# Optimization experiments

Hardware: AMD Instinct MI355X
Metric: run time of the kernel (lower is better)

The kernel has to match this reference:

```python
import jax, jax.numpy as jnp
import numpy as np
import math

B, S, N_STATE = 2, 2048, 2048
N_HEAD, D_HEAD = 16, 128
NEG = -1e9


def rope(x, f_r, f_i):
    # x: [B,S,H,D], f_*: [B,S,1,D//2]
    x_r, x_i = jnp.split(x, 2, axis=-1)
    return jnp.concatenate([x_r * f_r - x_i * f_i, x_r * f_i + x_i * f_r], axis=-1)


def setup_inputs() -> dict:
    key = jax.random.key(0)
    ks = jax.random.split(key, 6)
    x = jax.random.normal(ks[0], (B, S, N_STATE), jnp.float32)
    # rotary freqs: cos/sin of standard RoPE angles
    inv_freq = 1.0 / (10000.0 ** (jnp.arange(0, D_HEAD, 2, dtype=jnp.float32) / D_HEAD))
    ang = jnp.arange(S, dtype=jnp.float32)[:, None] * inv_freq[None, :]  # [S, D/2]
    f_r = jnp.broadcast_to(jnp.cos(ang)[None, :, None, :], (B, S, 1, D_HEAD // 2))
    f_i = jnp.broadcast_to(jnp.sin(ang)[None, :, None, :], (B, S, 1, D_HEAD // 2))
    # causal additive mask: 0 on/below diagonal, -1e9 above
    causal = jnp.where(jnp.tril(jnp.ones((S, S), bool)), 0.0, NEG).astype(jnp.float32)
    attention_mask = jnp.broadcast_to(causal[None], (B, S, S))
    std = 1.0 / math.sqrt(N_STATE)
    W_qkv = jax.random.normal(ks[1], (3 * N_HEAD * D_HEAD, N_STATE), jnp.float32) * std
    b_qkv = jax.random.normal(ks[2], (3 * N_HEAD * D_HEAD,), jnp.float32) * 0.02
    W_o = jax.random.normal(ks[3], (N_STATE, N_HEAD * D_HEAD), jnp.float32) * std
    return {"x": x, "f_r": f_r, "f_i": f_i, "attention_mask": attention_mask,
            "W_qkv": W_qkv, "b_qkv": b_qkv, "W_o": W_o}


def reference(x, f_r, f_i, attention_mask, W_qkv, b_qkv, W_o):
    nb, ns, _ = x.shape
    qkv = x @ W_qkv.T + b_qkv  # [B,S,3*H*D]
    q, k, v = jnp.split(qkv, 3, axis=-1)
    q = rope(q.reshape(nb, ns, N_HEAD, D_HEAD), f_r, f_i)
    k = rope(k.reshape(nb, ns, N_HEAD, D_HEAD), f_r, f_i)
    v = v.reshape(nb, ns, N_HEAD, D_HEAD)
    # kv_cache=None: cache is just (k, v)
    qk = jnp.einsum("bqhd,bkhd->bhqk", q, k) / math.sqrt(D_HEAD)
    qk = qk + attention_mask[:, None, :, :]
    scores = jax.nn.softmax(qk.astype(jnp.float32), axis=-1).astype(x.dtype)
    out = jnp.einsum("bhqk,bkhd->bqhd", scores, v).reshape(nb, ns, N_HEAD * D_HEAD)
    out = out @ W_o.T
    return out, k, v
```

## Files before the change

### kernel.cpp

```cpp
#include <hip/hip_runtime.h>
#include <stdint.h>

#define BS   2
#define SS   2048
#define NH   16
#define DH   128
#define HD   2048
#define KDIM 2048
#define NT   32

typedef _Float16 half_t;
typedef _Float16 half8 __attribute__((ext_vector_type(8)));
typedef _Float16 half4v __attribute__((ext_vector_type(4)));
typedef float   float4_ __attribute__((ext_vector_type(4)));

__device__ __forceinline__ void async16(const void* g, void* l) {
  __builtin_amdgcn_global_load_lds(
      (__attribute__((address_space(1))) void*)(void*)g,
      (__attribute__((address_space(3))) void*)l,
      16, 0, 0);
}

#define XN4  2097152
#define WQ4  3145728
#define WO4  1048576
__global__ __launch_bounds__(256) void conv_all(const float* __restrict__ x,
                                                const float* __restrict__ Wqkv,
                                                const float* __restrict__ Wo,
                                                half_t* __restrict__ xh,
                                                half_t* __restrict__ wqh,
                                                half_t* __restrict__ woh) {
  int i = blockIdx.x * 256 + threadIdx.x;
  const float* src; half_t* dst; int o;
  if (i < XN4)            { src = x;    dst = xh;  o = i; }
  else if (i < XN4 + WQ4) { src = Wqkv; dst = wqh; o = i - XN4; }
  else                    { src = Wo;   dst = woh; o = i - XN4 - WQ4; }
  float4 v = ((const float4*)src)[o];
  half4v hv;
  hv.x = (half_t)v.x; hv.y = (half_t)v.y; hv.z = (half_t)v.z; hv.w = (half_t)v.w;
  ((half4v*)dst)[o] = hv;
}


__device__ __forceinline__ const half8* lds_frag(const half_t* l, int row, int j) {
  return (const half8*)&l[(row * 8 + (j ^ (row & 7))) * 8];
}

__device__ __forceinline__ void stage8(const half_t* __restrict__ Ab,
                                       const half_t* __restrict__ Wb,
                                       half_t* dA, half_t* dB, int k0,
                                       int wave, int lane) {
#pragma unroll
  for (int i = 0; i < 4; ++i) {
    int p = (wave * 4 + i) * 64 + lane;
    int r = p >> 3, j = (p & 7) ^ ((p >> 3) & 7);
    async16(Ab + (size_t)r * KDIM + k0 + j * 8, &dA[p * 8]);
    async16(Wb + (size_t)r * KDIM + k0 + j * 8, &dB[p * 8]);
  }
}

__device__ __forceinline__ void gemm_core(const half_t* __restrict__ Ab,
                                          const half_t* __restrict__ Wb,
                                          half_t* lA, half_t* lB,
                                          float4_ acc[4][4]) {
  const int tid = threadIdx.x, wave = tid >> 6, lane = tid & 63;
  const int quad = lane >> 4, tl = lane & 15;
  const int wm = wave >> 1, wn = wave & 1;

  stage8(Ab, Wb, lA, lB, 0, wave, lane);
  stage8(Ab, Wb, lA + 8192, lB + 8192, 64, wave, lane);

  for (int t = 0; t < NT; ++t) {
    if (t == NT - 1) asm volatile("s_waitcnt vmcnt(0)" ::: "memory");
    else             asm volatile("s_waitcnt vmcnt(8)" ::: "memory");
    __builtin_amdgcn_s_barrier();

    const half_t* cA = lA + (t & 1) * 8192;
    const half_t* cB = lB + (t & 1) * 8192;
    half8 af[4][2], bf[4][2];
#pragma unroll
    for (int ks = 0; ks < 2; ++ks) {
#pragma unroll
      for (int mi = 0; mi < 4; ++mi)
        af[mi][ks] = *lds_frag(cA, wm * 64 + mi * 16 + tl, ks * 4 + quad);
#pragma unroll
      for (int ni = 0; ni < 4; ++ni)
        bf[ni][ks] = *lds_frag(cB, wn * 64 + ni * 16 + tl, ks * 4 + quad);
    }
    asm volatile("s_waitcnt lgkmcnt(0)" ::: "memory");
    __builtin_amdgcn_sched_barrier(0);
    __builtin_amdgcn_s_barrier();

    if (t + 2 < NT)
      stage8(Ab, Wb, lA + (t & 1) * 8192, lB + (t & 1) * 8192,
             (t + 2) * 64, wave, lane);
    __builtin_amdgcn_sched_barrier(0);

    __builtin_amdgcn_s_setprio(1);
#pragma unroll
    for (int mi = 0; mi < 4; ++mi)
#pragma unroll
      for (int ni = 0; ni < 4; ++ni)
#pragma unroll
        for (int ks = 0; ks < 2; ++ks)
          acc[mi][ni] = __builtin_amdgcn_mfma_f32_16x16x32_f16(
              af[mi][ks], bf[ni][ks], acc[mi][ni], 0, 0, 0);
    __builtin_amdgcn_s_setprio(0);
  }
}

__global__ __launch_bounds__(256) void gemm_qkv(const half_t* __restrict__ A,
                                                const half_t* __restrict__ W,
                                                const float* __restrict__ bias,
                                                half_t* __restrict__ qh,
                                                half_t* __restrict__ kh,
                                                half_t* __restrict__ vh,
                                                float* __restrict__ vout) {
  __shared__ __align__(16) half_t lA[2 * 128 * 64];
  __shared__ __align__(16) half_t lB[2 * 128 * 64];
  const int tid = threadIdx.x, wave = tid >> 6, lane = tid & 63;
  const int quad = lane >> 4, tl = lane & 15;
  const int wm = wave >> 1, wn = wave & 1;
  const int bm = blockIdx.y * 128, bn = blockIdx.x * 128;

  float4_ acc[4][4];
#pragma unroll
  for (int mi = 0; mi < 4; ++mi)
#pragma unroll
    for (int ni = 0; ni < 4; ++ni)
#pragma unroll
      for (int r = 0; r < 4; ++r) acc[mi][ni][r] = 0.f;

  gemm_core(A + (size_t)bm * KDIM, W + (size_t)bn * KDIM, lA, lB, acc);

#pragma unroll
  for (int mi = 0; mi < 4; ++mi) {
    int rowb = bm + wm * 64 + mi * 16 + quad * 4;
#pragma unroll
    for (int ni = 0; ni < 4; ++ni) {
      int col = bn + wn * 64 + ni * 16 + tl;
      float bv = bias[col];
#pragma unroll
      for (int r = 0; r < 4; ++r) {
        float v = acc[mi][ni][r] + bv;
        size_t off = (size_t)(rowb + r) * HD;
        if (col < 2048)       qh[off + col]        = (half_t)v;
        else if (col < 4096)  kh[off + col - 2048] = (half_t)v;
        else {
          vh[off + col - 4096]   = (half_t)v;
          vout[off + col - 4096] = v;
        }
      }
    }
  }
}

__global__ __launch_bounds__(256) void gemm_out(const half_t* __restrict__ A,
                                                const half_t* __restrict__ W,
                                                float* __restrict__ out) {
  __shared__ __align__(16) half_t lA[2 * 128 * 64];
  __shared__ __align__(16) half_t lB[2 * 128 * 64];
  const int tid = threadIdx.x, wave = tid >> 6, lane = tid & 63;
  const int quad = lane >> 4, tl = lane & 15;
  const int wm = wave >> 1, wn = wave & 1;
  const int bm = blockIdx.y * 128, bn = blockIdx.x * 128;

  float4_ acc[4][4];
#pragma unroll
  for (int mi = 0; mi < 4; ++mi)
#pragma unroll
    for (int ni = 0; ni < 4; ++ni)
#pragma unroll
      for (int r = 0; r < 4; ++r) acc[mi][ni][r] = 0.f;

  gemm_core(A + (size_t)bm * KDIM, W + (size_t)bn * KDIM, lA, lB, acc);

#pragma unroll
  for (int mi = 0; mi < 4; ++mi) {
    int rowb = bm + wm * 64 + mi * 16 + quad * 4;
#pragma unroll
    for (int ni = 0; ni < 4; ++ni) {
      int col = bn + wn * 64 + ni * 16 + tl;
#pragma unroll
      for (int r = 0; r < 4; ++r)
        out[(size_t)(rowb + r) * HD + col] = acc[mi][ni][r];
    }
  }
}

__global__ __launch_bounds__(256) void rope_vpost(half_t* __restrict__ qh,
                                                  half_t* __restrict__ kh,
                                                  const float* __restrict__ fr,
                                                  const float* __restrict__ fi,
                                                  float* __restrict__ kout,
                                                  const half_t* __restrict__ vh,
                                                  half_t* __restrict__ vt) {
  __shared__ half_t t[64 * 72];
  if (blockIdx.x < 2048) {
    int n = blockIdx.x * 256 + threadIdx.x;
    int u = n & 7;
    int h = (n >> 3) & 15;
    int s = (n >> 7) & 2047;
    int b = n >> 18;
    size_t row = (size_t)(b * SS + s);
    size_t base = row * HD + h * DH + u * 8;
    const float4_* fr4 = (const float4_*)(fr + row * 64 + u * 8);
    const float4_* fi4 = (const float4_*)(fi + row * 64 + u * 8);
    float4_ frv0 = fr4[0], frv1 = fr4[1];
    float4_ fiv0 = fi4[0], fiv1 = fi4[1];
    half8 qlo = *(const half8*)(qh + base), qhi = *(const half8*)(qh + base + 64);
    half8 klo = *(const half8*)(kh + base), khi = *(const half8*)(kh + base + 64);
    half8 qlo_o, qhi_o, klo_o, khi_o;
    float4_ kr0, kr1, ki0, ki1;
#pragma unroll
    for (int j = 0; j < 8; ++j) {
      float cr = (j < 4) ? frv0[j & 3] : frv1[j & 3];
      float ci = (j < 4) ? fiv0[j & 3] : fiv1[j & 3];
      float xr = (float)qlo[j], xi = (float)qhi[j];
      qlo_o[j] = (half_t)(xr * cr - xi * ci);
      qhi_o[j] = (half_t)(xr * ci + xi * cr);
      xr = (float)klo[j]; xi = (float)khi[j];
      float kr = xr * cr - xi * ci, ki = xr * ci + xi * cr;
      klo_o[j] = (half_t)kr; khi_o[j] = (half_t)ki;
      if (j < 4) { kr0[j & 3] = kr; ki0[j & 3] = ki; }
      else       { kr1[j & 3] = kr; ki1[j & 3] = ki; }
    }
    *(half8*)(qh + base)      = qlo_o;
    *(half8*)(qh + base + 64) = qhi_o;
    *(half8*)(kh + base)      = klo_o;
    *(half8*)(kh + base + 64) = khi_o;
    ((float4_*)(kout + base))[0]      = kr0;
    ((float4_*)(kout + base))[1]      = kr1;
    ((float4_*)(kout + base + 64))[0] = ki0;
    ((float4_*)(kout + base + 64))[1] = ki1;
  } else {
    int bid = blockIdx.x - 2048;
    int d0 = (bid & 1) * 64, s0 = ((bid >> 1) & 31) * 64, bh = bid >> 6;
    int b = bh >> 4, h = bh & 15;
#pragma unroll
    for (int it = 0; it < 2; ++it) {
      int e = it * 256 + threadIdx.x;
      int s = e >> 3, du = e & 7;
      half8 v = *(const half8*)(vh + (size_t)(b * SS + s0 + s) * HD + h * DH + d0 + du * 8);
#pragma unroll
      for (int j = 0; j < 8; ++j) t[(du * 8 + j) * 72 + s] = v[j];
    }
    __syncthreads();
#pragma unroll
    for (int it = 0; it < 2; ++it) {
      int e = it * 256 + threadIdx.x;
      int d = e >> 3, su = e & 7;
      half8 v;
#pragma unroll
      for (int j = 0; j < 8; ++j) v[j] = t[d * 72 + su * 8 + j];
      *(half8*)(vt + ((size_t)bh * DH + d0 + d) * SS + s0 + su * 8) = v;
    }
  }
}

#define SOFTMAX_SHIFT 2.0f

__device__ __forceinline__ void stage_kv(const half_t* __restrict__ khb,
                                         const half_t* __restrict__ vtb,
                                         half_t* dK, half_t* dV, int kt, int tid) {
#pragma unroll
  for (int i = 0; i < 2; ++i) {
    int p = i * 512 + tid;
    int rk = p >> 4, jk = (p & 15) ^ ((p >> 4) & 7);
    async16(khb + (size_t)(kt * 64 + rk) * HD + jk * 8, &dK[p * 8]);
    int rv = p >> 3, jv = (p & 7) ^ ((p >> 3) & 7);
    async16(vtb + (size_t)rv * SS + kt * 64 + jv * 8, &dV[p * 8]);
  }
}

__global__ __launch_bounds__(512) void attn_kernel(const half_t* __restrict__ qh,
                                                   const half_t* __restrict__ kh,
                                                   const half_t* __restrict__ vt,
                                                   half_t* __restrict__ oh) {
  __shared__ __align__(16) half_t lK[2 * 64 * 128];
  __shared__ __align__(16) half_t lV[2 * 128 * 64];
  __shared__ __align__(16) half_t lP[8 * 16 * 72];
  const int bid = blockIdx.x;
  const int bh = (bid & 7) * 4 + ((bid >> 3) & 3);
  const int qp = bid >> 5;
  const int b = bh >> 4, h = bh & 15;
  const int tid = threadIdx.x, wave = tid >> 6, lane = tid & 63;
  const int quad = lane >> 4, tl = lane & 15;
  const float scale = 0.08838834764831845f;

  half_t* myP = &lP[wave * 16 * 72];
  const half_t* qbase = qh + (size_t)(b * SS) * HD + h * DH;
  const half_t* khb   = kh + (size_t)(b * SS) * HD + h * DH;
  const half_t* vtb   = vt + (size_t)bh * DH * SS;

  for (int ph = 0; ph < 2; ++ph) {
    const int qt = ph ? (15 - qp) : qp;
    const int q0 = qt * 128 + wave * 16;
    const int nkt = 2 * qt + 2;

    half8 qf[4];
#pragma unroll
    for (int ks = 0; ks < 4; ++ks)
      qf[ks] = *(const half8*)(qbase + (size_t)(q0 + tl) * HD + ks * 32 + quad * 8);

    float4_ oacc[8];
#pragma unroll
    for (int t = 0; t < 8; ++t)
#pragma unroll
      for (int r = 0; r < 4; ++r) oacc[t][r] = 0.f;
    float lpart[4] = {0.f, 0.f, 0.f, 0.f};

    stage_kv(khb, vtb, lK, lV, 0, tid);

    for (int kt = 0; kt < nkt; ++kt) {
      const half_t* cK = lK + (kt & 1) * 8192;
      const half_t* cV = lV + (kt & 1) * 8192;
      if (kt + 1 < nkt) {
        stage_kv(khb, vtb, lK + ((kt + 1) & 1) * 8192, lV + ((kt + 1) & 1) * 8192,
                 kt + 1, tid);
        asm volatile("s_waitcnt vmcnt(4)" ::: "memory");
      } else {
        asm volatile("s_waitcnt vmcnt(0)" ::: "memory");
      }
      __builtin_amdgcn_s_barrier();
      __builtin_amdgcn_sched_barrier(0);

      float4_ sacc[4];
#pragma unroll
      for (int tn = 0; tn < 4; ++tn)
#pragma unroll
        for (int r = 0; r < 4; ++r) sacc[tn][r] = 0.f;
      __builtin_amdgcn_s_setprio(1);
#pragma unroll
      for (int ks = 0; ks < 4; ++ks) {
#pragma unroll
        for (int tn = 0; tn < 4; ++tn) {
          int row = tn * 16 + tl;
          int j = ks * 4 + quad;
          half8 kf = *(const half8*)&cK[(row * 16 + (j ^ (row & 7))) * 8];
          sacc[tn] = __builtin_amdgcn_mfma_f32_16x16x32_f16(qf[ks], kf, sacc[tn], 0, 0, 0);
        }
      }
      __builtin_amdgcn_s_setprio(0);

      if (kt * 64 + 63 > q0) {
#pragma unroll
        for (int tn = 0; tn < 4; ++tn) {
          int kvcol = kt * 64 + tn * 16 + tl;
#pragma unroll
          for (int j = 0; j < 4; ++j) {
            int qrow = q0 + quad * 4 + j;
            float sv = fmaf(sacc[tn][j], scale, -SOFTMAX_SHIFT);
            float pv = (kvcol > qrow) ? 0.f : __expf(sv);
            lpart[j] += pv;
            myP[(quad * 4 + j) * 72 + tn * 16 + tl] = (half_t)pv;
          }
        }
      } else {
#pragma unroll
        for (int tn = 0; tn < 4; ++tn)
#pragma unroll
          for (int j = 0; j < 4; ++j) {
            float pv = __expf(fmaf(sacc[tn][j], scale, -SOFTMAX_SHIFT));
            lpart[j] += pv;
            myP[(quad * 4 + j) * 72 + tn * 16 + tl] = (half_t)pv;
          }
      }

      __builtin_amdgcn_s_setprio(1);
#pragma unroll
      for (int ks2 = 0; ks2 < 2; ++ks2) {
        half8 pf = *(const half8*)&myP[tl * 72 + ks2 * 32 + quad * 8];
#pragma unroll
        for (int t = 0; t < 8; ++t) {
          int row = t * 16 + tl;
          int j = ks2 * 4 + quad;
          half8 vf = *(const half8*)&cV[(row * 8 + (j ^ (row & 7))) * 8];
          oacc[t] = __builtin_amdgcn_mfma_f32_16x16x32_f16(pf, vf, oacc[t], 0, 0, 0);
        }
      }
      __builtin_amdgcn_s_setprio(0);
      __builtin_amdgcn_s_barrier();
    }

#pragma unroll
    for (int off = 1; off <= 8; off <<= 1)
#pragma unroll
      for (int j = 0; j < 4; ++j)
        lpart[j] += __shfl_xor(lpart[j], off, 64);
    float inv[4];
#pragma unroll
    for (int j = 0; j < 4; ++j) inv[j] = 1.f / lpart[j];
#pragma unroll
    for (int t = 0; t < 8; ++t)
#pragma unroll
      for (int j = 0; j < 4; ++j)
        oh[(size_t)(b * SS + q0 + quad * 4 + j) * HD + h * DH + t * 16 + tl] =
            (half_t)(oacc[t][j] * inv[j]);
  }
}

extern "C" void kernel_launch(void* const* d_in, const int* in_sizes, int n_in,
                              void* d_out, int out_size, void* d_ws, size_t ws_size,
                              hipStream_t stream) {
  const float* x    = (const float*)d_in[0];
  const float* fr   = (const float*)d_in[1];
  const float* fi   = (const float*)d_in[2];
  const float* Wqkv = (const float*)d_in[4];
  const float* bqkv = (const float*)d_in[5];
  const float* Wo   = (const float*)d_in[6];

  float* out  = (float*)d_out;
  float* kout = out + 8388608;
  float* vout = out + 16777216;

  char* ws = (char*)d_ws;
  half_t* xh  = (half_t*)(ws);
  half_t* wqh = (half_t*)(ws + 16777216);
  half_t* woh = (half_t*)(ws + 41943040);
  half_t* qh  = (half_t*)(ws + 50331648);
  half_t* kh  = (half_t*)(ws + 67108864);
  half_t* vh  = (half_t*)(ws + 83886080);
  half_t* vt  = (half_t*)(ws + 100663296);
  half_t* oh  = (half_t*)(ws + 117440512);

  conv_all<<<24576, 256, 0, stream>>>(x, Wqkv, Wo, xh, wqh, woh);
  gemm_qkv<<<dim3(48, 32), 256, 0, stream>>>(xh, wqh, bqkv, qh, kh, vh, vout);
  rope_vpost<<<4096, 256, 0, stream>>>(qh, kh, fr, fi, kout, vh, vt);
  attn_kernel<<<256, 512, 0, stream>>>(qh, kh, vt, oh);
  gemm_out<<<dim3(16, 32), 256, 0, stream>>>(oh, woh, out);
}
```

Baseline: 427.0 us.

## Double attention KV tile to 128 keys and widen conversion to 8 elements

The attention kernel now stages 128-key K/V tiles per iteration instead of 64. This halves the number of barriers and pipeline steps. It processes the softmax/PV product in two 64-key halves that reuse the per-wave P buffer, with an lgkmcnt wait between them. LDS use doubles to 128KB for K/V, which may cut occupancy, and the diagonal tile now wastes more masked work. The fp32-to-fp16 conversion kernel also handles 8 elements per thread with half the blocks.

```diff
diff --git a/kernel.cpp b/kernel.cpp
--- a/kernel.cpp
+++ b/kernel.cpp
@@ -21,9 +21,9 @@
       16, 0, 0);
 }
 
-#define XN4  2097152
-#define WQ4  3145728
-#define WO4  1048576
+#define XN8  1048576
+#define WQ8  1572864
+#define WO8  524288
 __global__ __launch_bounds__(256) void conv_all(const float* __restrict__ x,
                                                 const float* __restrict__ Wqkv,
                                                 const float* __restrict__ Wo,
@@ -32,13 +32,15 @@
                                                 half_t* __restrict__ woh) {
   int i = blockIdx.x * 256 + threadIdx.x;
   const float* src; half_t* dst; int o;
-  if (i < XN4)            { src = x;    dst = xh;  o = i; }
-  else if (i < XN4 + WQ4) { src = Wqkv; dst = wqh; o = i - XN4; }
-  else                    { src = Wo;   dst = woh; o = i - XN4 - WQ4; }
-  float4 v = ((const float4*)src)[o];
-  half4v hv;
-  hv.x = (half_t)v.x; hv.y = (half_t)v.y; hv.z = (half_t)v.z; hv.w = (half_t)v.w;
-  ((half4v*)dst)[o] = hv;
+  if (i < XN8)            { src = x;    dst = xh;  o = i; }
+  else if (i < XN8 + WQ8) { src = Wqkv; dst = wqh; o = i - XN8; }
+  else                    { src = Wo;   dst = woh; o = i - XN8 - WQ8; }
+  float4 v0 = ((const float4*)src)[2 * o];
+  float4 v1 = ((const float4*)src)[2 * o + 1];
+  half8 hv;
+  hv[0] = (half_t)v0.x; hv[1] = (half_t)v0.y; hv[2] = (half_t)v0.z; hv[3] = (half_t)v0.w;
+  hv[4] = (half_t)v1.x; hv[5] = (half_t)v1.y; hv[6] = (half_t)v1.z; hv[7] = (half_t)v1.w;
+  ((half8*)dst)[o] = hv;
 }
 
 
@@ -264,12 +266,11 @@
                                          const half_t* __restrict__ vtb,
                                          half_t* dK, half_t* dV, int kt, int tid) {
 #pragma unroll
-  for (int i = 0; i < 2; ++i) {
+  for (int i = 0; i < 4; ++i) {
     int p = i * 512 + tid;
-    int rk = p >> 4, jk = (p & 15) ^ ((p >> 4) & 7);
-    async16(khb + (size_t)(kt * 64 + rk) * HD + jk * 8, &dK[p * 8]);
-    int rv = p >> 3, jv = (p & 7) ^ ((p >> 3) & 7);
-    async16(vtb + (size_t)rv * SS + kt * 64 + jv * 8, &dV[p * 8]);
+    int r = p >> 4, j = (p & 15) ^ ((p >> 4) & 7);
+    async16(khb + (size_t)(kt * 128 + r) * HD + j * 8, &dK[p * 8]);
+    async16(vtb + (size_t)r * SS + kt * 128 + j * 8, &dV[p * 8]);
   }
 }
 
@@ -277,8 +278,8 @@
                                                    const half_t* __restrict__ kh,
                                                    const half_t* __restrict__ vt,
                                                    half_t* __restrict__ oh) {
-  __shared__ __align__(16) half_t lK[2 * 64 * 128];
-  __shared__ __align__(16) half_t lV[2 * 128 * 64];
+  __shared__ __align__(16) half_t lK[2 * 128 * 128];
+  __shared__ __align__(16) half_t lV[2 * 128 * 128];
   __shared__ __align__(16) half_t lP[8 * 16 * 72];
   const int bid = blockIdx.x;
   const int bh = (bid & 7) * 4 + ((bid >> 3) & 3);
@@ -296,7 +297,7 @@
   for (int ph = 0; ph < 2; ++ph) {
     const int qt = ph ? (15 - qp) : qp;
     const int q0 = qt * 128 + wave * 16;
-    const int nkt = 2 * qt + 2;
+    const int nkt = qt + 1;
 
     half8 qf[4];
 #pragma unroll
@@ -313,28 +314,28 @@
     stage_kv(khb, vtb, lK, lV, 0, tid);
 
     for (int kt = 0; kt < nkt; ++kt) {
-      const half_t* cK = lK + (kt & 1) * 8192;
-      const half_t* cV = lV + (kt & 1) * 8192;
+      const half_t* cK = lK + (kt & 1) * 16384;
+      const half_t* cV = lV + (kt & 1) * 16384;
       if (kt + 1 < nkt) {
-        stage_kv(khb, vtb, lK + ((kt + 1) & 1) * 8192, lV + ((kt + 1) & 1) * 8192,
+        stage_kv(khb, vtb, lK + ((kt + 1) & 1) * 16384, lV + ((kt + 1) & 1) * 16384,
                  kt + 1, tid);
-        asm volatile("s_waitcnt vmcnt(4)" ::: "memory");
+        asm volatile("s_waitcnt vmcnt(8)" ::: "memory");
       } else {
         asm volatile("s_waitcnt vmcnt(0)" ::: "memory");
       }
       __builtin_amdgcn_s_barrier();
       __builtin_amdgcn_sched_barrier(0);
 
-      float4_ sacc[4];
-#pragma unroll
-      for (int tn = 0; tn < 4; ++tn)
+      float4_ sacc[8];
+#pragma unroll
+      for (int tn = 0; tn < 8; ++tn)
 #pragma unroll
         for (int r = 0; r < 4; ++r) sacc[tn][r] = 0.f;
       __builtin_amdgcn_s_setprio(1);
 #pragma unroll
       for (int ks = 0; ks < 4; ++ks) {
 #pragma unroll
-        for (int tn = 0; tn < 4; ++tn) {
+        for (int tn = 0; tn < 8; ++tn) {
           int row = tn * 16 + tl;
           int j = ks * 4 + quad;
           half8 kf = *(const half8*)&cK[(row * 16 + (j ^ (row & 7))) * 8];
@@ -343,43 +344,50 @@
       }
       __builtin_amdgcn_s_setprio(0);
 
-      if (kt * 64 + 63 > q0) {
-#pragma unroll
-        for (int tn = 0; tn < 4; ++tn) {
-          int kvcol = kt * 64 + tn * 16 + tl;
-#pragma unroll
-          for (int j = 0; j < 4; ++j) {
-            int qrow = q0 + quad * 4 + j;
-            float sv = fmaf(sacc[tn][j], scale, -SOFTMAX_SHIFT);
-            float pv = (kvcol > qrow) ? 0.f : __expf(sv);
-            lpart[j] += pv;
-            myP[(quad * 4 + j) * 72 + tn * 16 + tl] = (half_t)pv;
+      const bool diag = (kt * 128 + 127 > q0);
+#pragma unroll
+      for (int h2 = 0; h2 < 2; ++h2) {
+        if (diag) {
+#pragma unroll
+          for (int tn = 0; tn < 4; ++tn) {
+            int kvcol = kt * 128 + h2 * 64 + tn * 16 + tl;
+#pragma unroll
+            for (int j = 0; j < 4; ++j) {
+              int qrow = q0 + quad * 4 + j;
+              float sv = fmaf(sacc[h2 * 4 + tn][j], scale, -SOFTMAX_SHIFT);
+              float pv = (kvcol > qrow) ? 0.f : __expf(sv);
+              lpart[j] += pv;
+              myP[(quad * 4 + j) * 72 + tn * 16 + tl] = (half_t)pv;
+            }
+          }
+        } else {
+#pragma unroll
+          for (int tn = 0; tn < 4; ++tn)
+#pragma unroll
+            for (int j = 0; j < 4; ++j) {
+              float pv = __expf(fmaf(sacc[h2 * 4 + tn][j], scale, -SOFTMAX_SHIFT));
+              lpart[j] += pv;
+              myP[(quad * 4 + j) * 72 + tn * 16 + tl] = (half_t)pv;
+            }
+        }
+        asm volatile("s_waitcnt lgkmcnt(0)" ::: "memory");
+
+        __builtin_amdgcn_s_setprio(1);
+#pragma unroll
+        for (int ks2 = 0; ks2 < 2; ++ks2) {
+          half8 pf = *(const half8*)&myP[tl * 72 + ks2 * 32 + quad * 8];
+#pragma unroll
+          for (int t = 0; t < 8; ++t) {
+            int row = t * 16 + tl;
+            int j = h2 * 8 + ks2 * 4 + quad;
+            half8 vf = *(const half8*)&cV[(row * 16 + (j ^ (row & 7))) * 8];
+            oacc[t] = __builtin_amdgcn_mfma_f32_16x16x32_f16(pf, vf, oacc[t], 0, 0, 0);
           }
         }
-      } else {
-#pragma unroll
-        for (int tn = 0; tn < 4; ++tn)
-#pragma unroll
-          for (int j = 0; j < 4; ++j) {
-            float pv = __expf(fmaf(sacc[tn][j], scale, -SOFTMAX_SHIFT));
-            lpart[j] += pv;
-            myP[(quad * 4 + j) * 72 + tn * 16 + tl] = (half_t)pv;
-          }
+        __builtin_amdgcn_s_setprio(0);
+        if (h2 == 0)
+          asm volatile("s_waitcnt lgkmcnt(0)" ::: "memory");
       }
-
-      __builtin_amdgcn_s_setprio(1);
-#pragma unroll
-      for (int ks2 = 0; ks2 < 2; ++ks2) {
-        half8 pf = *(const half8*)&myP[tl * 72 + ks2 * 32 + quad * 8];
-#pragma unroll
-        for (int t = 0; t < 8; ++t) {
-          int row = t * 16 + tl;
-          int j = ks2 * 4 + quad;
-          half8 vf = *(const half8*)&cV[(row * 8 + (j ^ (row & 7))) * 8];
-          oacc[t] = __builtin_amdgcn_mfma_f32_16x16x32_f16(pf, vf, oacc[t], 0, 0, 0);
-        }
-      }
-      __builtin_amdgcn_s_setprio(0);
       __builtin_amdgcn_s_barrier();
     }
 
@@ -424,7 +432,7 @@
   half_t* vt  = (half_t*)(ws + 100663296);
   half_t* oh  = (half_t*)(ws + 117440512);
 
-  conv_all<<<24576, 256, 0, stream>>>(x, Wqkv, Wo, xh, wqh, woh);
+  conv_all<<<12288, 256, 0, stream>>>(x, Wqkv, Wo, xh, wqh, woh);
   gemm_qkv<<<dim3(48, 32), 256, 0, stream>>>(xh, wqh, bqkv, qh, kh, vh, vout);
   rope_vpost<<<4096, 256, 0, stream>>>(qh, kh, fr, fi, kout, vh, vt);
   attn_kernel<<<256, 512, 0, stream>>>(qh, kh, vt, oh);
```

Result: no change. 428.2 us (+0.3%).
